# Kernel optimization log

Hardware: AMD Instinct MI355X
Metric: run time of the kernel (lower is better)

The kernel has to match this reference:

```python
import jax, jax.numpy as jnp
import numpy as np

N = 100000
E = 1600000
G = 2048          # number of graphs in the batch
F_IN = 22
H = 64
OUT = 1
EPS = 1e-5


def setup_inputs() -> dict:
    key = jax.random.key(0)
    ks = jax.random.split(key, 12)
    x = jax.random.normal(ks[0], (N, F_IN), dtype=jnp.float32)
    edge_index = jax.random.randint(ks[1], (2, E), 0, N, dtype=jnp.int32)
    batch = jnp.sort(jax.random.randint(ks[2], (N,), 0, G, dtype=jnp.int32))
    def lin(k, fan_out, fan_in):
        s = 1.0 / np.sqrt(fan_in)
        return jax.random.uniform(k, (fan_out, fan_in), jnp.float32, -s, s)
    return {
        "x": x, "edge_index": edge_index, "batch": batch,
        "W1": lin(ks[3], H, F_IN), "b1": jnp.zeros((H,), jnp.float32),
        "g1": jnp.ones((H,), jnp.float32), "be1": jnp.zeros((H,), jnp.float32),
        "W2": lin(ks[4], H, H), "b2": jnp.zeros((H,), jnp.float32),
        "g2": jnp.ones((H,), jnp.float32), "be2": jnp.zeros((H,), jnp.float32),
        "fcw1": lin(ks[5], H // 2, H), "fcb1": jnp.zeros((H // 2,), jnp.float32),
        "fcw2": lin(ks[6], OUT, H // 2), "fcb2": jnp.zeros((OUT,), jnp.float32),
    }


def _gcn_conv(x, src, dst, W, b):
    # PyG GCNConv: linear transform, add self-loops, symmetric D^-1/2 A D^-1/2 aggregation, + bias
    h = x @ W.T                                   # [N, out]
    loops = jnp.arange(N, dtype=src.dtype)
    s = jnp.concatenate([src, loops])             # [E+N]
    d = jnp.concatenate([dst, loops])
    deg = jax.ops.segment_sum(jnp.ones_like(d, dtype=h.dtype), d, num_segments=N)
    dinv = jax.lax.rsqrt(deg)                     # deg >= 1 due to self-loops
    norm = dinv[s] * dinv[d]                      # [E+N]
    msg = h[s] * norm[:, None]                    # [E+N, out] gather
    out = jax.ops.segment_sum(msg, d, num_segments=N)  # scatter-add
    return out + b


def _batchnorm(x, g, be):
    mu = jnp.mean(x, axis=0)
    var = jnp.mean((x - mu) ** 2, axis=0)
    return g * (x - mu) * jax.lax.rsqrt(var + EPS) + be


def reference(x, edge_index, batch, W1, b1, g1, be1, W2, b2, g2, be2,
              fcw1, fcb1, fcw2, fcb2):
    src, dst = edge_index[0], edge_index[1]
    h = _gcn_conv(x, src, dst, W1, b1)
    h = jax.nn.relu(_batchnorm(h, g1, be1))       # dropout = identity (eval)
    h = _gcn_conv(h, src, dst, W2, b2)
    h = jax.nn.relu(_batchnorm(h, g2, be2))
    # global mean pool over graphs
    sums = jax.ops.segment_sum(h, batch, num_segments=G)            # [G, H]
    cnts = jax.ops.segment_sum(jnp.ones((N,), h.dtype), batch, num_segments=G)
    pooled = sums / jnp.maximum(cnts, 1.0)[:, None]
    z = jax.nn.relu(pooled @ fcw1.T + fcb1)
    return z @ fcw2.T + fcb2                      # [G, OUT]
```

## Files before the change

### kernel.cpp

```cpp
#include <hip/hip_runtime.h>

static constexpr int Nn  = 100000;
static constexpr int Ne  = 1600000;
static constexpr int Gg  = 2048;
static constexpr int Fin = 22;
static constexpr float EPSf = 1e-5f;

static constexpr int NP   = 250;
static constexpr int CH   = Ne / NP;
static constexpr int BSH  = 8;
static constexpr int NBkt = (Nn + 255) >> 8;
static constexpr int HPAD = ((NP * NBkt + 3) & ~3);

__global__ __launch_bounds__(256) void k_part1(const int* __restrict__ dst,
                                               int* __restrict__ hist) {
    __shared__ int h[NBkt];
    int tid = threadIdx.x;
    for (int b = tid; b < NBkt; b += 256) h[b] = 0;
    __syncthreads();
    int e0 = blockIdx.x * CH;
    for (int i = tid; i < CH; i += 256)
        atomicAdd(&h[dst[e0 + i] >> BSH], 1);
    __syncthreads();
    for (int b = tid; b < NBkt; b += 256)
        hist[blockIdx.x * NBkt + b] = h[b];
}

__global__ __launch_bounds__(256) void k_sum(const int* __restrict__ hist,
                                             int* __restrict__ tot) {
    __shared__ int sh[256];
    int b = blockIdx.x, tid = threadIdx.x;
    sh[tid] = (tid < NP) ? hist[tid * NBkt + b] : 0;
    __syncthreads();
    for (int off = 128; off; off >>= 1) {
        if (tid < off) sh[tid] += sh[tid + off];
        __syncthreads();
    }
    if (tid == 0) tot[b] = sh[0];
}

__global__ __launch_bounds__(512) void k_base(const int* __restrict__ tot,
                                              int* __restrict__ base, double* stats) {
    __shared__ int sh[512];
    int t = threadIdx.x;
    if (t < 256) stats[t] = 0.0;
    int v = (t < NBkt) ? tot[t] : 0;
    sh[t] = v;
    __syncthreads();
    for (int off = 1; off < 512; off <<= 1) {
        int a = (t >= off) ? sh[t - off] : 0;
        __syncthreads();
        sh[t] += a;
        __syncthreads();
    }
    if (t < NBkt) base[t] = sh[t] - v;
    if (t == 0) base[NBkt] = Ne;
}

__global__ __launch_bounds__(256) void k_off(int* __restrict__ hist,
                                             const int* __restrict__ base) {
    __shared__ int sh[256];
    int b = blockIdx.x, t = threadIdx.x;
    int v = (t < NP) ? hist[t * NBkt + b] : 0;
    sh[t] = v;
    __syncthreads();
    for (int off = 1; off < 256; off <<= 1) {
        int a = (t >= off) ? sh[t - off] : 0;
        __syncthreads();
        sh[t] += a;
        __syncthreads();
    }
    if (t < NP) hist[t * NBkt + b] = base[b] + sh[t] - v;
}

__global__ __launch_bounds__(256) void k_part2(const int* __restrict__ src,
                                               const int* __restrict__ dst,
                                               const int* __restrict__ hist,
                                               int* __restrict__ bucketed) {
    __shared__ int cur[NBkt];
    int tid = threadIdx.x;
    for (int b = tid; b < NBkt; b += 256) cur[b] = hist[blockIdx.x * NBkt + b];
    __syncthreads();
    int e0 = blockIdx.x * CH;
    for (int i = tid; i < CH; i += 256) {
        int e = e0 + i;
        int s = src[e], d = dst[e];
        int pos = atomicAdd(&cur[d >> BSH], 1);
        bucketed[pos] = s | ((d & 255) << 17);
    }
}

__global__ __launch_bounds__(256) void k_bfill(const int* __restrict__ base,
                                               const int* __restrict__ bucketed,
                                               int* __restrict__ csr_src,
                                               int* __restrict__ row_ptr,
                                               float* __restrict__ dinv) {
    __shared__ int ncnt[256];
    __shared__ int sc[256];
    __shared__ int cur[256];
    int b = blockIdx.x, tid = threadIdx.x;
    int e0 = base[b], e1 = base[b + 1];
    ncnt[tid] = 0;
    __syncthreads();
    for (int i = e0 + tid; i < e1; i += 256)
        atomicAdd(&ncnt[bucketed[i] >> 17], 1);
    __syncthreads();
    int v = ncnt[tid];
    sc[tid] = v;
    __syncthreads();
    for (int off = 1; off < 256; off <<= 1) {
        int a = (tid >= off) ? sc[tid - off] : 0;
        __syncthreads();
        sc[tid] += a;
        __syncthreads();
    }
    int excl = sc[tid] - v;
    int node = (b << BSH) + tid;
    if (node < Nn) {
        int r = e0 + excl;
        row_ptr[node] = r;
        cur[tid] = r;
        dinv[node] = rsqrtf(1.0f + (float)v);
    }
    if (b == NBkt - 1 && tid == 0) row_ptr[Nn] = Ne;
    __syncthreads();
    for (int i = e0 + tid; i < e1; i += 256) {
        int p = bucketed[i];
        int pos = atomicAdd(&cur[p >> 17], 1);
        csr_src[pos] = p & 0x1FFFF;
    }
}

__global__ void k_pad(const float* __restrict__ x, const float* __restrict__ dinv,
                      float* __restrict__ xp) {
    int idx = blockIdx.x * blockDim.x + threadIdx.x;
    if (idx >= Nn * 6) return;
    int n = idx / 6, q = idx - n * 6;
    float di = dinv[n];
    float4 v;
    int f0 = q * 4;
    const float* xr = x + n * Fin;
    v.x = (f0 + 0 < Fin) ? xr[f0 + 0] * di : 0.f;
    v.y = (f0 + 1 < Fin) ? xr[f0 + 1] * di : 0.f;
    v.z = (f0 + 2 < Fin) ? xr[f0 + 2] * di : 0.f;
    v.w = (f0 + 3 < Fin) ? xr[f0 + 3] * di : 0.f;
    ((float4*)xp)[idx] = v;
}

__global__ __launch_bounds__(256) void k_gather1(const int* __restrict__ row_ptr,
                                                 const int* __restrict__ csr_src,
                                                 const float* __restrict__ dinv,
                                                 const float* __restrict__ xp,
                                                 float* __restrict__ outp) {
    int idx = blockIdx.x * blockDim.x + threadIdx.x;
    if (idx >= Nn * 6) return;
    int n = idx / 6, q = idx - n * 6;
    const float4* h4 = (const float4*)xp;
    float di = dinv[n];
    float4 a0 = h4[n * 6 + q];
    float4 a1 = make_float4(0.f, 0.f, 0.f, 0.f);
    float4 a2 = make_float4(0.f, 0.f, 0.f, 0.f);
    float4 a3 = make_float4(0.f, 0.f, 0.f, 0.f);
    int e = row_ptr[n], e1 = row_ptr[n + 1];
    for (; e + 3 < e1; e += 4) {
        int s0 = csr_src[e], s1 = csr_src[e + 1], s2 = csr_src[e + 2], s3 = csr_src[e + 3];
        float4 v0 = h4[s0 * 6 + q];
        float4 v1 = h4[s1 * 6 + q];
        float4 v2 = h4[s2 * 6 + q];
        float4 v3 = h4[s3 * 6 + q];
        a0.x += v0.x; a0.y += v0.y; a0.z += v0.z; a0.w += v0.w;
        a1.x += v1.x; a1.y += v1.y; a1.z += v1.z; a1.w += v1.w;
        a2.x += v2.x; a2.y += v2.y; a2.z += v2.z; a2.w += v2.w;
        a3.x += v3.x; a3.y += v3.y; a3.z += v3.z; a3.w += v3.w;
    }
    for (; e < e1; e++) {
        int s = csr_src[e];
        float4 vv = h4[s * 6 + q];
        a0.x += vv.x; a0.y += vv.y; a0.z += vv.z; a0.w += vv.w;
    }
    float4 r;
    r.x = (a0.x + a1.x + a2.x + a3.x) * di;
    r.y = (a0.y + a1.y + a2.y + a3.y) * di;
    r.z = (a0.z + a1.z + a2.z + a3.z) * di;
    r.w = (a0.w + a1.w + a2.w + a3.w) * di;
    ((float4*)outp)[n * 6 + q] = r;
}

__global__ __launch_bounds__(256) void k_gemm1(const float* __restrict__ aggx,
                                               const float* __restrict__ W1,
                                               const float* __restrict__ b1,
                                               float* __restrict__ out) {
    __shared__ float Wl[64 * 23];
    __shared__ float Xl[4][24];
    int tid = threadIdx.x;
    for (int i = tid; i < 64 * Fin; i += 256) {
        int o = i / Fin, k = i % Fin;
        Wl[o * 23 + k] = W1[i];
    }
    int f = tid & 63, ln = tid >> 6;
    float bf = b1[f];
    for (int base = blockIdx.x * 4; base < Nn; base += gridDim.x * 4) {
        __syncthreads();
        if (tid < 24) {
            int r = tid / 6, q = tid - (tid / 6) * 6;
            if (base + r < Nn)
                *((float4*)&Xl[r][q * 4]) = ((const float4*)aggx)[(base + r) * 6 + q];
        }
        __syncthreads();
        int n = base + ln;
        if (n < Nn) {
            float s = bf;
            #pragma unroll
            for (int k = 0; k < Fin; k++) s += Xl[ln][k] * Wl[f * 23 + k];
            out[n * 64 + f] = s;
        }
    }
}

__global__ __launch_bounds__(256) void k_bnstats(const float* __restrict__ a, double* stats) {
    __shared__ float ssum[256], ssq[256];
    int tid = threadIdx.x;
    int f = tid & 63, ln = tid >> 6;
    float s = 0.f, q = 0.f;
    for (int n = blockIdx.x * 4 + ln; n < Nn; n += gridDim.x * 4) {
        float v = a[n * 64 + f];
        s += v;
        q += v * v;
    }
    ssum[tid] = s; ssq[tid] = q;
    __syncthreads();
    if (tid < 64) {
        s = ssum[tid] + ssum[tid + 64] + ssum[tid + 128] + ssum[tid + 192];
        q = ssq[tid] + ssq[tid + 64] + ssq[tid + 128] + ssq[tid + 192];
        atomicAdd(&stats[f], (double)s);
        atomicAdd(&stats[64 + f], (double)q);
    }
}

__global__ __launch_bounds__(256) void k_gemm2(const float* __restrict__ xin,
                                               const float* __restrict__ W2,
                                               const double* __restrict__ stats,
                                               const float* __restrict__ g,
                                               const float* __restrict__ be,
                                               const float* __restrict__ dinv,
                                               float* __restrict__ out) {
    __shared__ float Wl[64 * 65];
    __shared__ float Xl[4][64];
    int tid = threadIdx.x;
    for (int i = tid; i < 64 * 64; i += 256) {
        int o = i >> 6, k = i & 63;
        Wl[o * 65 + k] = W2[i];
    }
    int f = tid & 63, ln = tid >> 6;
    double mu = stats[f] / (double)Nn;
    double var = stats[64 + f] / (double)Nn - mu * mu;
    float sc = rsqrtf((float)var + EPSf) * g[f];
    float muf = (float)mu;
    float bef = be[f];
    for (int base = blockIdx.x * 4; base < Nn; base += gridDim.x * 4) {
        __syncthreads();
        int n = base + ln;
        if (n < Nn) {
            float v = (xin[n * 64 + f] - muf) * sc + bef;
            Xl[ln][f] = v > 0.f ? v : 0.f;
        }
        __syncthreads();
        if (n < Nn) {
            float s = 0.f;
            #pragma unroll
            for (int k = 0; k < 64; k++) s += Xl[ln][k] * Wl[f * 65 + k];
            out[n * 64 + f] = s * dinv[n];
        }
    }
}

__global__ __launch_bounds__(256) void k_gather2(const int* __restrict__ row_ptr,
                                                 const int* __restrict__ csr_src,
                                                 const float* __restrict__ dinv,
                                                 const float* __restrict__ h,
                                                 const float* __restrict__ bias,
                                                 float* __restrict__ out) {
    int idx = blockIdx.x * blockDim.x + threadIdx.x;
    if (idx >= Nn * 16) return;
    int n = idx >> 4, q = idx & 15;
    const float4* h4 = (const float4*)h;
    float di = dinv[n];
    float4 bv = ((const float4*)bias)[q];
    float4 a0 = h4[n * 16 + q];
    float4 a1 = make_float4(0.f, 0.f, 0.f, 0.f);
    float4 a2 = make_float4(0.f, 0.f, 0.f, 0.f);
    float4 a3 = make_float4(0.f, 0.f, 0.f, 0.f);
    int e = row_ptr[n], e1 = row_ptr[n + 1];
    for (; e + 3 < e1; e += 4) {
        int s0 = csr_src[e], s1 = csr_src[e + 1], s2 = csr_src[e + 2], s3 = csr_src[e + 3];
        float4 v0 = h4[s0 * 16 + q];
        float4 v1 = h4[s1 * 16 + q];
        float4 v2 = h4[s2 * 16 + q];
        float4 v3 = h4[s3 * 16 + q];
        a0.x += v0.x; a0.y += v0.y; a0.z += v0.z; a0.w += v0.w;
        a1.x += v1.x; a1.y += v1.y; a1.z += v1.z; a1.w += v1.w;
        a2.x += v2.x; a2.y += v2.y; a2.z += v2.z; a2.w += v2.w;
        a3.x += v3.x; a3.y += v3.y; a3.z += v3.z; a3.w += v3.w;
    }
    for (; e < e1; e++) {
        int s = csr_src[e];
        float4 vv = h4[s * 16 + q];
        a0.x += vv.x; a0.y += vv.y; a0.z += vv.z; a0.w += vv.w;
    }
    float4 r;
    r.x = (a0.x + a1.x + a2.x + a3.x) * di + bv.x;
    r.y = (a0.y + a1.y + a2.y + a3.y) * di + bv.y;
    r.z = (a0.z + a1.z + a2.z + a3.z) * di + bv.z;
    r.w = (a0.w + a1.w + a2.w + a3.w) * di + bv.w;
    ((float4*)out)[n * 16 + q] = r;
}

__global__ __launch_bounds__(64) void k_poolmlp(const float* __restrict__ a,
                                                const int* __restrict__ batch,
                                                const double* __restrict__ stats,
                                                const float* __restrict__ g,
                                                const float* __restrict__ be,
                                                const float* __restrict__ fcw1,
                                                const float* __restrict__ fcb1,
                                                const float* __restrict__ fcw2,
                                                const float* __restrict__ fcb2,
                                                float* __restrict__ out) {
    __shared__ float p[64];
    int gidx = blockIdx.x;
    int tid = threadIdx.x;
    int lo = 0, hi = Nn;
    while (lo < hi) { int m = (lo + hi) >> 1; if (batch[m] < gidx) lo = m + 1; else hi = m; }
    int start = lo;
    hi = Nn;
    while (lo < hi) { int m = (lo + hi) >> 1; if (batch[m] < gidx + 1) lo = m + 1; else hi = m; }
    int end = lo;
    double mu = stats[tid] / (double)Nn;
    double var = stats[64 + tid] / (double)Nn - mu * mu;
    float sc = rsqrtf((float)var + EPSf) * g[tid];
    float muf = (float)mu;
    float bef = be[tid];
    float s = 0.f;
    for (int n = start; n < end; n++) {
        float v = (a[n * 64 + tid] - muf) * sc + bef;
        s += v > 0.f ? v : 0.f;
    }
    int cnt = end - start;
    float c = cnt < 1 ? 1.f : (float)cnt;
    p[tid] = s / c;
    __syncthreads();
    float w = 0.f;
    if (tid < 32) {
        float z = fcb1[tid];
        #pragma unroll
        for (int k = 0; k < 64; k++) z += p[k] * fcw1[tid * 64 + k];
        z = z > 0.f ? z : 0.f;
        w = z * fcw2[tid];
    }
    for (int off = 16; off; off >>= 1) w += __shfl_down(w, off);
    if (tid == 0) out[gidx] = w + fcb2[0];
}

extern "C" void kernel_launch(void* const* d_in, const int* in_sizes, int n_in,
                              void* d_out, int out_size, void* d_ws, size_t ws_size,
                              hipStream_t stream) {
    const float* x    = (const float*)d_in[0];
    const int* ei     = (const int*)d_in[1];
    const int* src    = ei;
    const int* dst    = ei + Ne;
    const int* batch  = (const int*)d_in[2];
    const float* W1   = (const float*)d_in[3];
    const float* b1   = (const float*)d_in[4];
    const float* g1   = (const float*)d_in[5];
    const float* be1  = (const float*)d_in[6];
    const float* W2   = (const float*)d_in[7];
    const float* b2   = (const float*)d_in[8];
    const float* g2   = (const float*)d_in[9];
    const float* be2  = (const float*)d_in[10];
    const float* fcw1 = (const float*)d_in[11];
    const float* fcb1 = (const float*)d_in[12];
    const float* fcw2 = (const float*)d_in[13];
    const float* fcb2 = (const float*)d_in[14];
    float* out = (float*)d_out;

    double* stats1   = (double*)d_ws;
    double* stats2   = stats1 + 128;
    int*    hist     = (int*)(stats1 + 256);
    int*    tot      = hist + HPAD;
    int*    base     = tot + 392;
    int*    bucketed = base + 392;
    int*    csr_src  = bucketed + Ne;
    int*    row_ptr  = csr_src + Ne;
    float*  dinv     = (float*)(row_ptr + 100004);
    float*  bufA     = dinv + Nn;
    float*  bufB     = bufA + Nn * 64;

    k_part1<<<NP, 256, 0, stream>>>(dst, hist);
    k_sum<<<NBkt, 256, 0, stream>>>(hist, tot);
    k_base<<<1, 512, 0, stream>>>(tot, base, stats1);
    k_off<<<NBkt, 256, 0, stream>>>(hist, base);
    k_part2<<<NP, 256, 0, stream>>>(src, dst, hist, bucketed);
    k_bfill<<<NBkt, 256, 0, stream>>>(base, bucketed, csr_src, row_ptr, dinv);

    k_pad<<<(Nn * 6 + 255) / 256, 256, 0, stream>>>(x, dinv, bufA);

    k_gather1<<<(Nn * 6 + 255) / 256, 256, 0, stream>>>(row_ptr, csr_src, dinv, bufA, bufB);
    k_gemm1<<<1024, 256, 0, stream>>>(bufB, W1, b1, bufA);
    k_bnstats<<<512, 256, 0, stream>>>(bufA, stats1);

    k_gemm2<<<2048, 256, 0, stream>>>(bufA, W2, stats1, g1, be1, dinv, bufB);
    k_gather2<<<(Nn * 16 + 255) / 256, 256, 0, stream>>>(row_ptr, csr_src, dinv, bufB, b2, bufA);
    k_bnstats<<<512, 256, 0, stream>>>(bufA, stats2);

    k_poolmlp<<<Gg, 64, 0, stream>>>(bufA, batch, stats2, g2, be2,
                                     fcw1, fcb1, fcw2, fcb2, out);
}
```

Before: 402.4 us.

## Fuse BatchNorm statistics into gemm1 and gather2, and pad layer-1 rows to 32 floats

```diff
diff --git a/kernel.cpp b/kernel.cpp
--- a/kernel.cpp
+++ b/kernel.cpp
@@ -134,16 +134,16 @@
 __global__ void k_pad(const float* __restrict__ x, const float* __restrict__ dinv,
                       float* __restrict__ xp) {
     int idx = blockIdx.x * blockDim.x + threadIdx.x;
-    if (idx >= Nn * 6) return;
-    int n = idx / 6, q = idx - n * 6;
+    if (idx >= Nn * 8) return;
+    int n = idx >> 3, q = idx & 7;
     float di = dinv[n];
-    float4 v;
+    float4 v = make_float4(0.f, 0.f, 0.f, 0.f);
     int f0 = q * 4;
     const float* xr = x + n * Fin;
-    v.x = (f0 + 0 < Fin) ? xr[f0 + 0] * di : 0.f;
-    v.y = (f0 + 1 < Fin) ? xr[f0 + 1] * di : 0.f;
-    v.z = (f0 + 2 < Fin) ? xr[f0 + 2] * di : 0.f;
-    v.w = (f0 + 3 < Fin) ? xr[f0 + 3] * di : 0.f;
+    if (f0 + 0 < Fin) v.x = xr[f0 + 0] * di;
+    if (f0 + 1 < Fin) v.y = xr[f0 + 1] * di;
+    if (f0 + 2 < Fin) v.z = xr[f0 + 2] * di;
+    if (f0 + 3 < Fin) v.w = xr[f0 + 3] * di;
     ((float4*)xp)[idx] = v;
 }
 
@@ -157,17 +157,17 @@
     int n = idx / 6, q = idx - n * 6;
     const float4* h4 = (const float4*)xp;
     float di = dinv[n];
-    float4 a0 = h4[n * 6 + q];
+    float4 a0 = h4[n * 8 + q];
     float4 a1 = make_float4(0.f, 0.f, 0.f, 0.f);
     float4 a2 = make_float4(0.f, 0.f, 0.f, 0.f);
     float4 a3 = make_float4(0.f, 0.f, 0.f, 0.f);
     int e = row_ptr[n], e1 = row_ptr[n + 1];
     for (; e + 3 < e1; e += 4) {
         int s0 = csr_src[e], s1 = csr_src[e + 1], s2 = csr_src[e + 2], s3 = csr_src[e + 3];
-        float4 v0 = h4[s0 * 6 + q];
-        float4 v1 = h4[s1 * 6 + q];
-        float4 v2 = h4[s2 * 6 + q];
-        float4 v3 = h4[s3 * 6 + q];
+        float4 v0 = h4[s0 * 8 + q];
+        float4 v1 = h4[s1 * 8 + q];
+        float4 v2 = h4[s2 * 8 + q];
+        float4 v3 = h4[s3 * 8 + q];
         a0.x += v0.x; a0.y += v0.y; a0.z += v0.z; a0.w += v0.w;
         a1.x += v1.x; a1.y += v1.y; a1.z += v1.z; a1.w += v1.w;
         a2.x += v2.x; a2.y += v2.y; a2.z += v2.z; a2.w += v2.w;
@@ -175,7 +175,7 @@
     }
     for (; e < e1; e++) {
         int s = csr_src[e];
-        float4 vv = h4[s * 6 + q];
+        float4 vv = h4[s * 8 + q];
         a0.x += vv.x; a0.y += vv.y; a0.z += vv.z; a0.w += vv.w;
     }
     float4 r;
@@ -189,9 +189,11 @@
 __global__ __launch_bounds__(256) void k_gemm1(const float* __restrict__ aggx,
                                                const float* __restrict__ W1,
                                                const float* __restrict__ b1,
-                                               float* __restrict__ out) {
+                                               float* __restrict__ out,
+                                               double* stats) {
     __shared__ float Wl[64 * 23];
     __shared__ float Xl[4][24];
+    __shared__ float r1[256], r2[256];
     int tid = threadIdx.x;
     for (int i = tid; i < 64 * Fin; i += 256) {
         int o = i / Fin, k = i % Fin;
@@ -199,6 +201,7 @@
     }
     int f = tid & 63, ln = tid >> 6;
     float bf = b1[f];
+    float ssum = 0.f, ssq = 0.f;
     for (int base = blockIdx.x * 4; base < Nn; base += gridDim.x * 4) {
         __syncthreads();
         if (tid < 24) {
@@ -213,27 +216,17 @@
             #pragma unroll
             for (int k = 0; k < Fin; k++) s += Xl[ln][k] * Wl[f * 23 + k];
             out[n * 64 + f] = s;
-        }
-    }
-}
-
-__global__ __launch_bounds__(256) void k_bnstats(const float* __restrict__ a, double* stats) {
-    __shared__ float ssum[256], ssq[256];
-    int tid = threadIdx.x;
-    int f = tid & 63, ln = tid >> 6;
-    float s = 0.f, q = 0.f;
-    for (int n = blockIdx.x * 4 + ln; n < Nn; n += gridDim.x * 4) {
-        float v = a[n * 64 + f];
-        s += v;
-        q += v * v;
-    }
-    ssum[tid] = s; ssq[tid] = q;
+            ssum += s;
+            ssq += s * s;
+        }
+    }
+    r1[tid] = ssum; r2[tid] = ssq;
     __syncthreads();
     if (tid < 64) {
-        s = ssum[tid] + ssum[tid + 64] + ssum[tid + 128] + ssum[tid + 192];
-        q = ssq[tid] + ssq[tid + 64] + ssq[tid + 128] + ssq[tid + 192];
-        atomicAdd(&stats[f], (double)s);
-        atomicAdd(&stats[64 + f], (double)q);
+        float s4 = r1[tid] + r1[tid + 64] + r1[tid + 128] + r1[tid + 192];
+        float q4 = r2[tid] + r2[tid + 64] + r2[tid + 128] + r2[tid + 192];
+        atomicAdd(&stats[tid], (double)s4);
+        atomicAdd(&stats[64 + tid], (double)q4);
     }
 }
 
@@ -279,40 +272,65 @@
                                                  const float* __restrict__ dinv,
                                                  const float* __restrict__ h,
                                                  const float* __restrict__ bias,
-                                                 float* __restrict__ out) {
-    int idx = blockIdx.x * blockDim.x + threadIdx.x;
-    if (idx >= Nn * 16) return;
-    int n = idx >> 4, q = idx & 15;
+                                                 float* __restrict__ out,
+                                                 double* stats) {
+    __shared__ float ss[64], sq[64];
+    int tid = threadIdx.x;
+    if (tid < 64) { ss[tid] = 0.f; sq[tid] = 0.f; }
+    __syncthreads();
     const float4* h4 = (const float4*)h;
-    float di = dinv[n];
-    float4 bv = ((const float4*)bias)[q];
-    float4 a0 = h4[n * 16 + q];
-    float4 a1 = make_float4(0.f, 0.f, 0.f, 0.f);
-    float4 a2 = make_float4(0.f, 0.f, 0.f, 0.f);
-    float4 a3 = make_float4(0.f, 0.f, 0.f, 0.f);
-    int e = row_ptr[n], e1 = row_ptr[n + 1];
-    for (; e + 3 < e1; e += 4) {
-        int s0 = csr_src[e], s1 = csr_src[e + 1], s2 = csr_src[e + 2], s3 = csr_src[e + 3];
-        float4 v0 = h4[s0 * 16 + q];
-        float4 v1 = h4[s1 * 16 + q];
-        float4 v2 = h4[s2 * 16 + q];
-        float4 v3 = h4[s3 * 16 + q];
-        a0.x += v0.x; a0.y += v0.y; a0.z += v0.z; a0.w += v0.w;
-        a1.x += v1.x; a1.y += v1.y; a1.z += v1.z; a1.w += v1.w;
-        a2.x += v2.x; a2.y += v2.y; a2.z += v2.z; a2.w += v2.w;
-        a3.x += v3.x; a3.y += v3.y; a3.z += v3.z; a3.w += v3.w;
-    }
-    for (; e < e1; e++) {
-        int s = csr_src[e];
-        float4 vv = h4[s * 16 + q];
-        a0.x += vv.x; a0.y += vv.y; a0.z += vv.z; a0.w += vv.w;
-    }
-    float4 r;
-    r.x = (a0.x + a1.x + a2.x + a3.x) * di + bv.x;
-    r.y = (a0.y + a1.y + a2.y + a3.y) * di + bv.y;
-    r.z = (a0.z + a1.z + a2.z + a3.z) * di + bv.z;
-    r.w = (a0.w + a1.w + a2.w + a3.w) * di + bv.w;
-    ((float4*)out)[n * 16 + q] = r;
+    float st0 = 0.f, st1 = 0.f, st2 = 0.f, st3 = 0.f;
+    float sg0 = 0.f, sg1 = 0.f, sg2 = 0.f, sg3 = 0.f;
+    for (int idx = blockIdx.x * 256 + tid; idx < Nn * 16; idx += gridDim.x * 256) {
+        int n = idx >> 4, q = idx & 15;
+        float di = dinv[n];
+        float4 bv = ((const float4*)bias)[q];
+        float4 a0 = h4[n * 16 + q];
+        float4 a1 = make_float4(0.f, 0.f, 0.f, 0.f);
+        float4 a2 = make_float4(0.f, 0.f, 0.f, 0.f);
+        float4 a3 = make_float4(0.f, 0.f, 0.f, 0.f);
+        int e = row_ptr[n], e1 = row_ptr[n + 1];
+        for (; e + 3 < e1; e += 4) {
+            int s0 = csr_src[e], s1 = csr_src[e + 1], s2 = csr_src[e + 2], s3 = csr_src[e + 3];
+            float4 v0 = h4[s0 * 16 + q];
+            float4 v1 = h4[s1 * 16 + q];
+            float4 v2 = h4[s2 * 16 + q];
+            float4 v3 = h4[s3 * 16 + q];
+            a0.x += v0.x; a0.y += v0.y; a0.z += v0.z; a0.w += v0.w;
+            a1.x += v1.x; a1.y += v1.y; a1.z += v1.z; a1.w += v1.w;
+            a2.x += v2.x; a2.y += v2.y; a2.z += v2.z; a2.w += v2.w;
+            a3.x += v3.x; a3.y += v3.y; a3.z += v3.z; a3.w += v3.w;
+        }
+        for (; e < e1; e++) {
+            int s = csr_src[e];
+            float4 vv = h4[s * 16 + q];
+            a0.x += vv.x; a0.y += vv.y; a0.z += vv.z; a0.w += vv.w;
+        }
+        float4 r;
+        r.x = (a0.x + a1.x + a2.x + a3.x) * di + bv.x;
+        r.y = (a0.y + a1.y + a2.y + a3.y) * di + bv.y;
+        r.z = (a0.z + a1.z + a2.z + a3.z) * di + bv.z;
+        r.w = (a0.w + a1.w + a2.w + a3.w) * di + bv.w;
+        ((float4*)out)[idx] = r;
+        st0 += r.x; sg0 += r.x * r.x;
+        st1 += r.y; sg1 += r.y * r.y;
+        st2 += r.z; sg2 += r.z * r.z;
+        st3 += r.w; sg3 += r.w * r.w;
+    }
+    int q = tid & 15;
+    atomicAdd(&ss[q * 4 + 0], st0);
+    atomicAdd(&ss[q * 4 + 1], st1);
+    atomicAdd(&ss[q * 4 + 2], st2);
+    atomicAdd(&ss[q * 4 + 3], st3);
+    atomicAdd(&sq[q * 4 + 0], sg0);
+    atomicAdd(&sq[q * 4 + 1], sg1);
+    atomicAdd(&sq[q * 4 + 2], sg2);
+    atomicAdd(&sq[q * 4 + 3], sg3);
+    __syncthreads();
+    if (tid < 64) {
+        atomicAdd(&stats[tid], (double)ss[tid]);
+        atomicAdd(&stats[64 + tid], (double)sq[tid]);
+    }
 }
 
 __global__ __launch_bounds__(64) void k_poolmlp(const float* __restrict__ a,
@@ -401,15 +419,13 @@
     k_part2<<<NP, 256, 0, stream>>>(src, dst, hist, bucketed);
     k_bfill<<<NBkt, 256, 0, stream>>>(base, bucketed, csr_src, row_ptr, dinv);
 
-    k_pad<<<(Nn * 6 + 255) / 256, 256, 0, stream>>>(x, dinv, bufA);
+    k_pad<<<(Nn * 8 + 255) / 256, 256, 0, stream>>>(x, dinv, bufA);
 
     k_gather1<<<(Nn * 6 + 255) / 256, 256, 0, stream>>>(row_ptr, csr_src, dinv, bufA, bufB);
-    k_gemm1<<<1024, 256, 0, stream>>>(bufB, W1, b1, bufA);
-    k_bnstats<<<512, 256, 0, stream>>>(bufA, stats1);
+    k_gemm1<<<1024, 256, 0, stream>>>(bufB, W1, b1, bufA, stats1);
 
     k_gemm2<<<2048, 256, 0, stream>>>(bufA, W2, stats1, g1, be1, dinv, bufB);
-    k_gather2<<<(Nn * 16 + 255) / 256, 256, 0, stream>>>(row_ptr, csr_src, dinv, bufB, b2, bufA);
-    k_bnstats<<<512, 256, 0, stream>>>(bufA, stats2);
+    k_gather2<<<1024, 256, 0, stream>>>(row_ptr, csr_src, dinv, bufB, b2, bufA, stats2);
 
     k_poolmlp<<<Gg, 64, 0, stream>>>(bufA, batch, stats2, g2, be2,
                                      fcw1, fcb1, fcw2, fcb2, out);
```

Result: no change. 401.2 us (-0.3%).
